# Kernel tuning notes

Measured on AMD Instinct MI355X. Metric: run time of the kernel, lower is better.

The kernel has to match this reference:

```python
import jax, jax.numpy as jnp
import numpy as np

N = 10000      # nodes
E = 160000     # edges
K = 32         # MC samples (dim 1 of inputs)
D_IN = 128
D_OUT = 32


def setup_inputs() -> dict:
    key = jax.random.key(0)
    k1, k2, k3, k4, k5 = jax.random.split(key, 5)
    x = jax.random.normal(k1, (N, K, D_IN), dtype=jnp.float32)
    # Glorot-uniform weight as in weight_variable_glorot
    init_range = np.sqrt(6.0 / (D_IN + D_OUT))
    weights = jax.random.uniform(k2, (D_IN, D_OUT), dtype=jnp.float32,
                                 minval=-init_range, maxval=init_range)
    edge_row = jax.random.randint(k3, (E,), 0, N, dtype=jnp.int32)
    edge_col = jax.random.randint(k4, (E,), 0, N, dtype=jnp.int32)
    edge_val = jax.random.uniform(k5, (E,), dtype=jnp.float32)
    return {"x": x, "weights": weights, "edge_row": edge_row,
            "edge_col": edge_col, "edge_val": edge_val}


def reference(x, weights, edge_row, edge_col, edge_val):
    # Original loops over K slices doing: dropout(p=0) -> x @ W -> spmm(adj, x) -> relu,
    # then concatenates along axis 1. Batched equivalent:
    h = jnp.einsum('nkd,de->nke', x, weights)            # [N, K, D_OUT]
    # sparse adj @ h : out[r] += val * h[c] for each edge (r, c, val)
    msg = h[edge_col] * edge_val[:, None, None]          # [E, K, D_OUT]
    agg = jax.ops.segment_sum(msg, edge_row, num_segments=N)  # [N, K, D_OUT]
    return jax.nn.relu(agg)
```

## Files before the change

### kernel.cpp

```cpp
#include <hip/hip_runtime.h>
#include <hip/hip_bf16.h>

#define KK 32
#define DIN 128
#define DOUT 32
#define NVEC (KK * DOUT)
#define MBKT 64
#define OCAP 4096

typedef float        vf4    __attribute__((ext_vector_type(4)));
typedef unsigned int vu4    __attribute__((ext_vector_type(4)));
typedef short        bf16x8 __attribute__((ext_vector_type(8)));

__device__ __forceinline__ float bfu2f(unsigned int u) {
    return __uint_as_float(u << 16);
}
__device__ __forceinline__ unsigned int f2bfu(float f) {
    __hip_bfloat16 b = __float2bfloat16(f);
    return *(unsigned short*)&b;
}

__global__ __launch_bounds__(256) void prep_kernel(
    int* __restrict__ p, int n,
    const float* __restrict__ w, unsigned short* __restrict__ wfrag)
{
    int i = blockIdx.x * 256 + threadIdx.x;
    if (i < n) p[i] = 0;
    if (blockIdx.x == 0) {
        for (int item = threadIdx.x; item < 512; item += 256) {
            int lane = item & 63;
            int fk   = item >> 6;
            int nt   = fk >> 2, ks = fk & 3;
            int q    = lane >> 4, lm = lane & 15;
            #pragma unroll
            for (int j = 0; j < 8; ++j) {
                int k = ks * 32 + q * 8 + j;
                wfrag[(size_t)item * 8 + j] =
                    (unsigned short)f2bfu(w[k * DOUT + nt * 16 + lm]);
            }
        }
    }
}

__global__ __launch_bounds__(256) void gemm_fill_kernel(
    const float* __restrict__ x, const unsigned short* __restrict__ wfrag,
    unsigned short* __restrict__ h,
    const int* __restrict__ erow, const int* __restrict__ ecol,
    const float* __restrict__ eval, int* __restrict__ cursor,
    uint2* __restrict__ bedge,
    int* __restrict__ ocnt, int* __restrict__ orow,
    int* __restrict__ ocol, float* __restrict__ oval,
    int E, int FB)
{
    const int tid = threadIdx.x;

    if (blockIdx.x < (unsigned)FB) {
        int i = blockIdx.x * 256 + tid;
        if (i >= E) return;
        int r = __builtin_nontemporal_load(erow + i);
        int p = atomicAdd(&cursor[r], 1);
        if (p < MBKT) {
            uint2 e;
            e.x = (unsigned int)__builtin_nontemporal_load(ecol + i);
            e.y = __float_as_uint(__builtin_nontemporal_load(eval + i));
            bedge[r * MBKT + p] = e;
        } else {
            int q = atomicAdd(ocnt, 1);
            if (q < OCAP) {
                orow[q] = r;
                ocol[q] = ecol[i];
                oval[q] = eval[i];
            }
        }
        return;
    }

    const int lane = tid & 63;
    const int wid  = tid >> 6;
    const int q    = lane >> 4;
    const int lm   = lane & 15;

    bf16x8 bf[2][4];
    {
        const bf16x8* wf = (const bf16x8*)wfrag;
        #pragma unroll
        for (int nt = 0; nt < 2; ++nt)
            #pragma unroll
            for (int ks = 0; ks < 4; ++ks)
                bf[nt][ks] = wf[(nt * 4 + ks) * 64 + lane];
    }

    const int tile = (blockIdx.x - FB) * 4 + wid;
    const int r0   = tile * 16;
    const float* xrow = x + (size_t)(r0 + lm) * DIN + q * 8;

    vf4 acc0 = {0.f, 0.f, 0.f, 0.f};
    vf4 acc1 = {0.f, 0.f, 0.f, 0.f};

    #pragma unroll
    for (int ks = 0; ks < 4; ++ks) {
        vf4 a0 = __builtin_nontemporal_load((const vf4*)(xrow + ks * 32));
        vf4 a1 = __builtin_nontemporal_load((const vf4*)(xrow + ks * 32 + 4));
        bf16x8 af;
        af[0] = (short)f2bfu(a0.x); af[1] = (short)f2bfu(a0.y);
        af[2] = (short)f2bfu(a0.z); af[3] = (short)f2bfu(a0.w);
        af[4] = (short)f2bfu(a1.x); af[5] = (short)f2bfu(a1.y);
        af[6] = (short)f2bfu(a1.z); af[7] = (short)f2bfu(a1.w);
        acc0 = __builtin_amdgcn_mfma_f32_16x16x32_bf16(af, bf[0][ks], acc0, 0, 0, 0);
        acc1 = __builtin_amdgcn_mfma_f32_16x16x32_bf16(af, bf[1][ks], acc1, 0, 0, 0);
    }

    #pragma unroll
    for (int q2 = 0; q2 < 4; ++q2) {
        unsigned int pk = f2bfu(acc0[q2]) | (f2bfu(acc1[q2]) << 16);
        *(unsigned int*)(h + (size_t)(r0 + q * 4 + q2) * DOUT + lm * 2) = pk;
    }
}

__global__ __launch_bounds__(128) void agg_kernel(
    const unsigned short* __restrict__ h, const int* __restrict__ cursor,
    const uint2* __restrict__ bedge,
    const int* __restrict__ ocnt, const int* __restrict__ orow,
    const int* __restrict__ ocol, const float* __restrict__ oval,
    float* __restrict__ out)
{
    const int lt   = threadIdx.x;
    const int lane = lt & 63;
    const int r    = blockIdx.x;

    const int deg  = cursor[r];
    const int degb = deg < MBKT ? deg : MBKT;
    const int on0  = *ocnt;

    int   ec = 0;
    float ev = 0.f;
    if (lane < degb) {
        uint2 e = bedge[r * MBKT + lane];
        ec = (int)e.x;
        ev = __uint_as_float(e.y);
    }

    float acc[8];
    #pragma unroll
    for (int q = 0; q < 8; ++q) acc[q] = 0.f;

    #pragma unroll 8
    for (int j = 0; j < degb; ++j) {
        int   c = __shfl(ec, j, 64);
        float v = __shfl(ev, j, 64);
        vu4 p = *(const vu4*)(h + (size_t)c * NVEC + lt * 8);
        acc[0] += v * bfu2f(p.x & 0xffffu);
        acc[1] += v * bfu2f(p.x >> 16);
        acc[2] += v * bfu2f(p.y & 0xffffu);
        acc[3] += v * bfu2f(p.y >> 16);
        acc[4] += v * bfu2f(p.z & 0xffffu);
        acc[5] += v * bfu2f(p.z >> 16);
        acc[6] += v * bfu2f(p.w & 0xffffu);
        acc[7] += v * bfu2f(p.w >> 16);
    }

    if (on0 > 0) {
        int on = on0 > OCAP ? OCAP : on0;
        for (int q = 0; q < on; ++q) {
            if (orow[q] == r) {
                int   c = ocol[q];
                float v = oval[q];
                vu4 p = *(const vu4*)(h + (size_t)c * NVEC + lt * 8);
                acc[0] += v * bfu2f(p.x & 0xffffu);
                acc[1] += v * bfu2f(p.x >> 16);
                acc[2] += v * bfu2f(p.y & 0xffffu);
                acc[3] += v * bfu2f(p.y >> 16);
                acc[4] += v * bfu2f(p.z & 0xffffu);
                acc[5] += v * bfu2f(p.z >> 16);
                acc[6] += v * bfu2f(p.w & 0xffffu);
                acc[7] += v * bfu2f(p.w >> 16);
            }
        }
    }

    vf4 oA, oB;
    oA.x = fmaxf(acc[0], 0.f); oA.y = fmaxf(acc[2], 0.f);
    oA.z = fmaxf(acc[4], 0.f); oA.w = fmaxf(acc[6], 0.f);
    oB.x = fmaxf(acc[1], 0.f); oB.y = fmaxf(acc[3], 0.f);
    oB.z = fmaxf(acc[5], 0.f); oB.w = fmaxf(acc[7], 0.f);
    float* obase = out + (size_t)r * NVEC + (lt >> 2) * 32 + (lt & 3) * 4;
    __builtin_nontemporal_store(oA, (vf4*)obase);
    __builtin_nontemporal_store(oB, (vf4*)(obase + 16));
}

extern "C" void kernel_launch(void* const* d_in, const int* in_sizes, int n_in,
                              void* d_out, int out_size, void* d_ws, size_t ws_size,
                              hipStream_t stream)
{
    const float* x    = (const float*)d_in[0];
    const float* w    = (const float*)d_in[1];
    const int*   erow = (const int*)d_in[2];
    const int*   ecol = (const int*)d_in[3];
    const float* eval = (const float*)d_in[4];
    float* out = (float*)d_out;

    const int E = in_sizes[2];
    const int N = in_sizes[0] / (KK * DIN);
    const int R = N * KK;

    char* ws = (char*)d_ws;
    size_t off = 0;
    auto take = [&](size_t bytes) {
        void* p = ws + off;
        off += (bytes + 15) & ~(size_t)15;
        return p;
    };
    unsigned short* h = (unsigned short*)take((size_t)R * DOUT * sizeof(unsigned short));
    int*   cursor = (int*)take((size_t)(N + 1) * sizeof(int));
    uint2* bedge  = (uint2*)take((size_t)N * MBKT * sizeof(uint2));
    int*   orow   = (int*)take((size_t)OCAP * sizeof(int));
    int*   ocol   = (int*)take((size_t)OCAP * sizeof(int));
    float* oval   = (float*)take((size_t)OCAP * sizeof(float));
    unsigned short* wfrag = (unsigned short*)take((size_t)512 * 8 * sizeof(unsigned short));
    int*   ocnt   = cursor + N;
    (void)ws_size;

    const int FB = (E + 255) / 256;
    const int GB = (R / 16) / 4;

    prep_kernel<<<(N + 1 + 255) / 256, 256, 0, stream>>>(cursor, N + 1, w, wfrag);
    gemm_fill_kernel<<<FB + GB, 256, 0, stream>>>(
        x, wfrag, h, erow, ecol, eval, cursor, bedge, ocnt, orow, ocol, oval, E, FB);
    agg_kernel<<<N, 128, 0, stream>>>(
        h, cursor, bedge, ocnt, orow, ocol, oval, out);
}
```

Baseline: 299.9 us.

## Split h into per-column-group slabs and parallelize aggregation across edges

The GEMM writes h in a slab layout grouped by 4 K-samples, so each node's slice per group is a contiguous 256-byte chunk. The aggregation kernel now launches 8 column-group blocks per pair of rows, with one wave per row and four 16-lane groups processing different edges concurrently, then reduces across the groups with shuffles. This aims to shrink the gather working set per group for better cache reuse and to raise memory-level parallelism on low-degree rows. In exchange, the edge lists are re-read per group and extra shuffle reductions are added.

```diff
diff --git a/kernel.cpp b/kernel.cpp
--- a/kernel.cpp
+++ b/kernel.cpp
@@ -10,6 +10,7 @@
 
 typedef float        vf4    __attribute__((ext_vector_type(4)));
 typedef unsigned int vu4    __attribute__((ext_vector_type(4)));
+typedef unsigned int vu2    __attribute__((ext_vector_type(2)));
 typedef short        bf16x8 __attribute__((ext_vector_type(8)));
 
 __device__ __forceinline__ float bfu2f(unsigned int u) {
@@ -44,13 +45,13 @@
 
 __global__ __launch_bounds__(256) void gemm_fill_kernel(
     const float* __restrict__ x, const unsigned short* __restrict__ wfrag,
-    unsigned short* __restrict__ h,
+    unsigned short* __restrict__ h2,
     const int* __restrict__ erow, const int* __restrict__ ecol,
     const float* __restrict__ eval, int* __restrict__ cursor,
     uint2* __restrict__ bedge,
     int* __restrict__ ocnt, int* __restrict__ orow,
     int* __restrict__ ocol, float* __restrict__ oval,
-    int E, int FB)
+    int E, int FB, int NN)
 {
     const int tid = threadIdx.x;
 
@@ -110,23 +111,32 @@
         acc1 = __builtin_amdgcn_mfma_f32_16x16x32_bf16(af, bf[1][ks], acc1, 0, 0, 0);
     }
 
+    const int n  = tile >> 1;
+    const int cc = tile & 1;
+    unsigned short* hbase =
+        h2 + ((size_t)(4 * cc + q) * NN + n) * 128 + lm * 2;
     #pragma unroll
     for (int q2 = 0; q2 < 4; ++q2) {
         unsigned int pk = f2bfu(acc0[q2]) | (f2bfu(acc1[q2]) << 16);
-        *(unsigned int*)(h + (size_t)(r0 + q * 4 + q2) * DOUT + lm * 2) = pk;
+        *(unsigned int*)(hbase + q2 * 32) = pk;
     }
 }
 
 __global__ __launch_bounds__(128) void agg_kernel(
-    const unsigned short* __restrict__ h, const int* __restrict__ cursor,
+    const unsigned short* __restrict__ h2, const int* __restrict__ cursor,
     const uint2* __restrict__ bedge,
     const int* __restrict__ ocnt, const int* __restrict__ orow,
     const int* __restrict__ ocol, const float* __restrict__ oval,
-    float* __restrict__ out)
-{
-    const int lt   = threadIdx.x;
-    const int lane = lt & 63;
-    const int r    = blockIdx.x;
+    float* __restrict__ out, int N)
+{
+    const int tid  = threadIdx.x;
+    const int wv   = tid >> 6;
+    const int lane = tid & 63;
+    const int li   = lane & 15;
+    const int eg   = lane >> 4;
+    const int g    = blockIdx.x & 7;
+    const int r    = (blockIdx.x >> 3) * 2 + wv;
+    if (r >= N) return;
 
     const int deg  = cursor[r];
     const int degb = deg < MBKT ? deg : MBKT;
@@ -135,20 +145,24 @@
     int   ec = 0;
     float ev = 0.f;
     if (lane < degb) {
-        uint2 e = bedge[r * MBKT + lane];
+        vu2 e = __builtin_nontemporal_load((const vu2*)bedge + r * MBKT + lane);
         ec = (int)e.x;
         ev = __uint_as_float(e.y);
     }
 
+    const unsigned short* hg = h2 + (size_t)g * N * 128;
+
     float acc[8];
     #pragma unroll
     for (int q = 0; q < 8; ++q) acc[q] = 0.f;
 
-    #pragma unroll 8
-    for (int j = 0; j < degb; ++j) {
-        int   c = __shfl(ec, j, 64);
-        float v = __shfl(ev, j, 64);
-        vu4 p = *(const vu4*)(h + (size_t)c * NVEC + lt * 8);
+    const int iters = (degb + 3) >> 2;
+    #pragma unroll 4
+    for (int j = 0; j < iters; ++j) {
+        int   idx = j * 4 + eg;
+        int   c = __shfl(ec, idx, 64);
+        float v = __shfl(ev, idx, 64);
+        vu4 p = *(const vu4*)(hg + (size_t)c * 128 + li * 8);
         acc[0] += v * bfu2f(p.x & 0xffffu);
         acc[1] += v * bfu2f(p.x >> 16);
         acc[2] += v * bfu2f(p.y & 0xffffu);
@@ -159,13 +173,19 @@
         acc[7] += v * bfu2f(p.w >> 16);
     }
 
+    #pragma unroll
+    for (int q = 0; q < 8; ++q) {
+        acc[q] += __shfl_xor(acc[q], 16, 64);
+        acc[q] += __shfl_xor(acc[q], 32, 64);
+    }
+
     if (on0 > 0) {
         int on = on0 > OCAP ? OCAP : on0;
         for (int q = 0; q < on; ++q) {
             if (orow[q] == r) {
                 int   c = ocol[q];
                 float v = oval[q];
-                vu4 p = *(const vu4*)(h + (size_t)c * NVEC + lt * 8);
+                vu4 p = *(const vu4*)(hg + (size_t)c * 128 + li * 8);
                 acc[0] += v * bfu2f(p.x & 0xffffu);
                 acc[1] += v * bfu2f(p.x >> 16);
                 acc[2] += v * bfu2f(p.y & 0xffffu);
@@ -178,14 +198,17 @@
         }
     }
 
-    vf4 oA, oB;
-    oA.x = fmaxf(acc[0], 0.f); oA.y = fmaxf(acc[2], 0.f);
-    oA.z = fmaxf(acc[4], 0.f); oA.w = fmaxf(acc[6], 0.f);
-    oB.x = fmaxf(acc[1], 0.f); oB.y = fmaxf(acc[3], 0.f);
-    oB.z = fmaxf(acc[5], 0.f); oB.w = fmaxf(acc[7], 0.f);
-    float* obase = out + (size_t)r * NVEC + (lt >> 2) * 32 + (lt & 3) * 4;
-    __builtin_nontemporal_store(oA, (vf4*)obase);
-    __builtin_nontemporal_store(oB, (vf4*)(obase + 16));
+    if (eg == 0) {
+        vf4 oA, oB;
+        oA.x = fmaxf(acc[0], 0.f); oA.y = fmaxf(acc[2], 0.f);
+        oA.z = fmaxf(acc[4], 0.f); oA.w = fmaxf(acc[6], 0.f);
+        oB.x = fmaxf(acc[1], 0.f); oB.y = fmaxf(acc[3], 0.f);
+        oB.z = fmaxf(acc[5], 0.f); oB.w = fmaxf(acc[7], 0.f);
+        float* obase = out + (size_t)r * NVEC
+                     + (4 * g + (li >> 2)) * 32 + (li & 3) * 4;
+        __builtin_nontemporal_store(oA, (vf4*)obase);
+        __builtin_nontemporal_store(oB, (vf4*)(obase + 16));
+    }
 }
 
 extern "C" void kernel_launch(void* const* d_in, const int* in_sizes, int n_in,
@@ -225,7 +248,8 @@
 
     prep_kernel<<<(N + 1 + 255) / 256, 256, 0, stream>>>(cursor, N + 1, w, wfrag);
     gemm_fill_kernel<<<FB + GB, 256, 0, stream>>>(
-        x, wfrag, h, erow, ecol, eval, cursor, bedge, ocnt, orow, ocol, oval, E, FB);
-    agg_kernel<<<N, 128, 0, stream>>>(
-        h, cursor, bedge, ocnt, orow, ocol, oval, out);
-}
+        x, wfrag, h, erow, ecol, eval, cursor, bedge, ocnt, orow, ocol, oval,
+        E, FB, N);
+    agg_kernel<<<((N + 1) / 2) * 8, 128, 0, stream>>>(
+        h, cursor, bedge, ocnt, orow, ocol, oval, out, N);
+}
```

Result: no change. 304.7 us (+1.6%).
